# Performance work log

Hardware: AMD Instinct MI355X
Metric: run time of the kernel (lower is better)

Reference implementation:

```python
import jax, jax.numpy as jnp
import numpy as np

N = 1
IN_C = 256
NUM_ANCHORS = 9
NUM_CLASSES = 91
# (H, W, stride) per FPN level for an 800x800 input
LEVELS = [(100, 100, 8), (50, 50, 16), (25, 25, 32), (13, 13, 64), (7, 7, 128)]
BBOX_CLAMP = float(np.log(1000.0 / 16.0))


def setup_inputs() -> dict:
    key = jax.random.key(0)
    ks = jax.random.split(key, 12)
    std = 0.01
    inp = {}
    for i, (h, w, _) in enumerate(LEVELS):
        inp[f"feat{i}"] = jax.random.normal(ks[i], (N, IN_C, h, w), jnp.float32)
    inp["cls_tw"] = jax.random.normal(ks[5], (4, IN_C, IN_C, 3, 3), jnp.float32) * std
    inp["cls_tb"] = jnp.zeros((4, IN_C), jnp.float32)
    inp["cls_out_w"] = jax.random.normal(ks[6], (NUM_ANCHORS * NUM_CLASSES, IN_C, 3, 3), jnp.float32) * std
    # prior-probability bias init: -log((1-p)/p) with p=0.01
    inp["cls_out_b"] = jnp.full((NUM_ANCHORS * NUM_CLASSES,), -np.log((1 - 0.01) / 0.01), jnp.float32)
    inp["reg_tw"] = jax.random.normal(ks[7], (4, IN_C, IN_C, 3, 3), jnp.float32) * std
    inp["reg_tb"] = jnp.zeros((4, IN_C), jnp.float32)
    inp["reg_out_w"] = jax.random.normal(ks[8], (NUM_ANCHORS * 4, IN_C, 3, 3), jnp.float32) * std
    inp["reg_out_b"] = jnp.zeros((NUM_ANCHORS * 4,), jnp.float32)
    return inp


def _conv3(x, w, b):
    y = jax.lax.conv_general_dilated(x, w, (1, 1), [(1, 1), (1, 1)],
                                     dimension_numbers=("NCHW", "OIHW", "NCHW"))
    return y + b[None, :, None, None]


def _run_head(feat, tw, tb, ow, ob, K):
    x = feat
    for i in range(4):  # fixed 4-layer tower
        x = jax.nn.relu(_conv3(x, tw[i], tb[i]))
    y = _conv3(x, ow, ob)                      # [N, A*K, H, W]
    n, _, h, w = y.shape
    y = y.reshape(n, -1, K, h, w)              # [N, A, K, H, W]
    y = jnp.transpose(y, (0, 3, 4, 1, 2))      # [N, H, W, A, K]
    return y.reshape(n, -1, K)                 # [N, H*W*A, K]


def _make_anchors():
    base_sizes = [32.0, 64.0, 128.0, 256.0, 512.0]
    scales = np.array([2 ** (i / 3.0) for i in range(3)], np.float32)
    ratios = np.array([0.5, 1.0, 2.0], np.float32)
    h_ratios = np.sqrt(ratios)
    w_ratios = 1.0 / h_ratios
    out = []
    for lvl, (H, W, stride) in enumerate(LEVELS):
        sizes = base_sizes[lvl] * scales                      # [3]
        ws = (w_ratios[:, None] * sizes[None, :]).reshape(-1)  # [9], ratio-major
        hs = (h_ratios[:, None] * sizes[None, :]).reshape(-1)
        base = np.stack([-ws, -hs, ws, hs], axis=1) / 2.0      # [9, 4]
        sy = np.arange(H, dtype=np.float32) * stride
        sx = np.arange(W, dtype=np.float32) * stride
        yy, xx = np.meshgrid(sy, sx, indexing="ij")
        shifts = np.stack([xx, yy, xx, yy], axis=-1).reshape(-1, 4)  # [H*W, 4]
        out.append((shifts[:, None, :] + base[None, :, :]).reshape(-1, 4))
    return jnp.asarray(np.concatenate(out, axis=0))  # [A_total, 4]


def _decode(reg, anchors):
    # torchvision BoxCoder.decode with weights (1,1,1,1)
    aw = anchors[:, 2] - anchors[:, 0]
    ah = anchors[:, 3] - anchors[:, 1]
    acx = anchors[:, 0] + 0.5 * aw
    acy = anchors[:, 1] + 0.5 * ah
    dx, dy, dw, dh = reg[..., 0], reg[..., 1], reg[..., 2], reg[..., 3]
    dw = jnp.minimum(dw, BBOX_CLAMP)
    dh = jnp.minimum(dh, BBOX_CLAMP)
    pcx = dx * aw + acx
    pcy = dy * ah + acy
    pw = jnp.exp(dw) * aw
    ph = jnp.exp(dh) * ah
    return jnp.stack([pcx - 0.5 * pw, pcy - 0.5 * ph, pcx + 0.5 * pw, pcy + 0.5 * ph], axis=-1)


def reference(feat0, feat1, feat2, feat3, feat4,
              cls_tw, cls_tb, cls_out_w, cls_out_b,
              reg_tw, reg_tb, reg_out_w, reg_out_b):
    feats = [feat0, feat1, feat2, feat3, feat4]
    cls_logits = jnp.concatenate(
        [_run_head(f, cls_tw, cls_tb, cls_out_w, cls_out_b, NUM_CLASSES) for f in feats], axis=1)
    bbox_reg = jnp.concatenate(
        [_run_head(f, reg_tw, reg_tb, reg_out_w, reg_out_b, 4) for f in feats], axis=1)
    anchors = _make_anchors()                     # [A_total, 4]
    boxes = _decode(bbox_reg, anchors)            # [N, A_total, 4]
    scores = jax.nn.sigmoid(cls_logits)           # [N, A_total, 91]
    return jnp.concatenate([scores, boxes], axis=-1)  # [N, A_total, 95]
```

## Files before the change

kernel.cpp:

```cpp
#include <hip/hip_runtime.h>
#include <math.h>

typedef unsigned short u16;
typedef __attribute__((ext_vector_type(8))) short s8v;
typedef __attribute__((ext_vector_type(4))) float f4v;

#define NUM_CLASSES 91
#define NUM_ANCHORS 9
#define NT2 247
#define TG8 31
#define TW_STRIDE (256*256*9)
#define PSTRIDE 872

struct Tab {
    int tstart[5];
    int tw[5];
    int H[5], W[5], GP0[5];
};

__device__ __forceinline__ u16 f2bf(float f) {
    unsigned u = __float_as_uint(f);
    u += 0x7fffu + ((u >> 16) & 1u);
    return (u16)(u >> 16);
}

__global__ __launch_bounds__(256) void conv2bf_all(
    const float* __restrict__ f0, const float* __restrict__ f1,
    const float* __restrict__ f2, const float* __restrict__ f3,
    const float* __restrict__ f4, u16* __restrict__ out, Tab tab)
{
    int gp = blockIdx.x * 64 + (threadIdx.x & 63);
    int cg = threadIdx.x >> 6;
    if (gp >= 13343) return;
    int lvl = 0;
    if (gp >= tab.GP0[1]) lvl = 1;
    if (gp >= tab.GP0[2]) lvl = 2;
    if (gp >= tab.GP0[3]) lvl = 3;
    if (gp >= tab.GP0[4]) lvl = 4;
    const float* x = lvl == 0 ? f0 : lvl == 1 ? f1 : lvl == 2 ? f2 : lvl == 3 ? f3 : f4;
    int p = gp - tab.GP0[lvl];
    int HW = tab.H[lvl] * tab.W[lvl];
    #pragma unroll
    for (int pass = 0; pass < 8; ++pass) {
        int c0 = pass * 32 + cg * 8;
        s8v v8;
        #pragma unroll
        for (int j = 0; j < 8; ++j)
            v8[j] = (short)f2bf(x[(c0 + j) * HW + p]);
        *(s8v*)(out + (((size_t)gp << 8) + c0)) = v8;
    }
}

__device__ __forceinline__ void pack_one(const float* __restrict__ w,
                                         u16* __restrict__ dst,
                                         int idx, int c_out_real)
{
    int lane = idx & 63;
    int t2 = idx >> 6;
    int chunk = t2 % 72;
    int co16 = t2 / 72;
    int tap = chunk >> 3, cib = chunk & 7;
    int co = co16 * 16 + (lane & 15);
    int ci0 = cib * 32 + ((lane >> 4) << 3);
    s8v v8;
    #pragma unroll
    for (int j = 0; j < 8; ++j) {
        float v = (co < c_out_real) ? w[((co << 8) + ci0 + j) * 9 + tap] : 0.f;
        v8[j] = (short)f2bf(v);
    }
    *(s8v*)(dst + (size_t)idx * 8) = v8;
}

__global__ __launch_bounds__(256) void pack_all(
    const float* __restrict__ cls_tw, const float* __restrict__ reg_tw,
    const float* __restrict__ cls_ow, const float* __restrict__ reg_ow,
    u16* __restrict__ pt, size_t pt_stride_u16,
    u16* __restrict__ pc, u16* __restrict__ pr)
{
    int idx = blockIdx.x * 256 + threadIdx.x;
    const int per_t = 72 * 16 * 64;
    const int cls_n = 72 * 52 * 64;
    const int reg_n = 72 * 3 * 64;
    if (idx < 8 * per_t) {
        int layer = idx / per_t;
        int r = idx - layer * per_t;
        const float* src = (layer < 4) ? cls_tw + (size_t)layer * TW_STRIDE
                                       : reg_tw + (size_t)(layer - 4) * TW_STRIDE;
        pack_one(src, pt + (size_t)layer * pt_stride_u16, r, 256);
    } else if (idx < 8 * per_t + cls_n) {
        pack_one(cls_ow, pc, idx - 8 * per_t, 819);
    } else if (idx < 8 * per_t + cls_n + reg_n) {
        pack_one(reg_ow, pr, idx - 8 * per_t - cls_n, 36);
    }
}

__global__ __launch_bounds__(256) void pack_w(const float* __restrict__ w,
                                              u16* __restrict__ dst,
                                              int c_out_real, int nco16)
{
    int idx = blockIdx.x * 256 + threadIdx.x;
    if (idx < 72 * nco16 * 64) pack_one(w, dst, idx, c_out_real);
}

template<int MODE, int NCO16, int ACCN>
__device__ __forceinline__ void conv_core(
    u16* __restrict__ lds,
    const u16* __restrict__ act, const u16* __restrict__ wpk,
    const float* __restrict__ bias,
    u16* __restrict__ outw, float* __restrict__ fout,
    int bx, int by, const Tab& tab)
{
    int lvl = 0;
    if (by >= tab.tstart[1]) lvl = 1;
    if (by >= tab.tstart[2]) lvl = 2;
    if (by >= tab.tstart[3]) lvl = 3;
    if (by >= tab.tstart[4]) lvl = 4;
    const int H = tab.H[lvl], W = tab.W[lvl], gp0 = tab.GP0[lvl];
    const int t = by - tab.tstart[lvl];
    const int tw = tab.tw[lvl];
    const int w0 = (t % tw) * 16;
    const int h0 = (t / tw) * 4;

    const int tid = threadIdx.x;
    const int lane = tid & 63, wv = tid >> 6;
    const int co16w = bx * (4 * ACCN) + wv * ACCN;
    const int kg = lane >> 4;
    const int col = lane & 15;

    int sofs[4], slds[4];
    bool svalid[4], slive[4];
    #pragma unroll
    for (int i = 0; i < 4; ++i) {
        int k = tid + i * 256;
        slive[i] = k < 864;
        int kk = slive[i] ? k : 0;
        int px = kk >> 3, part = kk & 7;
        int hh = px / 18, ww = px - hh * 18;
        int gh = h0 + hh - 1, gw = w0 + ww - 1;
        svalid[i] = ((unsigned)gh < (unsigned)H) && ((unsigned)gw < (unsigned)W);
        sofs[i] = ((gp0 + gh * W + gw) << 8) + part * 8;
        slds[i] = part * PSTRIDE + px * 8;
    }

    const u16* bbn[ACCN];
    #pragma unroll
    for (int n = 0; n < ACCN; ++n) {
        int c = co16w + n;
        if (c >= NCO16) c = NCO16 - 1;
        bbn[n] = wpk + ((size_t)(c * 72) << 9) + (lane << 3);
    }

    f4v acc[4][ACCN];
    #pragma unroll
    for (int s = 0; s < 4; ++s)
        #pragma unroll
        for (int n = 0; n < ACCN; ++n)
            acc[s][n] = (f4v){0.f, 0.f, 0.f, 0.f};

    s8v pre[4];
    auto ISSUE_S = [&](int cc) {
        #pragma unroll
        for (int i = 0; i < 4; ++i) {
            s8v v = {};
            if (slive[i] && svalid[i])
                v = *(const s8v*)(act + sofs[i] + cc * 64);
            pre[i] = v;
        }
    };

    ISSUE_S(0);
    #pragma unroll 1
    for (int cib = 0; cib < 4; ++cib) {
        if (cib) __syncthreads();
        #pragma unroll
        for (int i = 0; i < 4; ++i)
            if (slive[i]) *(s8v*)(&lds[slds[i]]) = pre[i];
        __syncthreads();

        #pragma unroll
        for (int cs = 0; cs < 2; ++cs) {
            const u16* L = &lds[(cs * 4 + kg) * PSTRIDE];
            #pragma unroll
            for (int kx = 0; kx < 3; ++kx) {
                s8v a[6];
                #pragma unroll
                for (int r = 0; r < 6; ++r)
                    a[r] = *(const s8v*)(&L[(r * 18 + col + kx) * 8]);
                #pragma unroll
                for (int ky = 0; ky < 3; ++ky) {
                    s8v b[ACCN];
                    #pragma unroll
                    for (int n = 0; n < ACCN; ++n)
                        b[n] = *(const s8v*)(bbn[n] +
                            ((size_t)((ky * 3 + kx) * 8 + cib * 2 + cs) << 9));
                    #pragma unroll
                    for (int s = 0; s < 4; ++s)
                        #pragma unroll
                        for (int n = 0; n < ACCN; ++n)
                            acc[s][n] = __builtin_amdgcn_mfma_f32_16x16x32_bf16(
                                a[s + ky], b[n], acc[s][n], 0, 0, 0);
                }
                if (cs == 0 && kx == 0 && cib < 3) ISSUE_S(cib + 1);
            }
        }
    }

    #pragma unroll
    for (int n = 0; n < ACCN; ++n) {
        const int co = (co16w + n) * 16 + (lane & 15);
        if (co < NCO16 * 16) {
            #pragma unroll
            for (int s = 0; s < 4; ++s) {
                const int h = h0 + s;
                #pragma unroll
                for (int j = 0; j < 4; ++j) {
                    const int w = w0 + ((lane >> 4) << 2) + j;
                    if (h < H && w < W) {
                        const int p = h * W + w;
                        if (MODE == 0) {
                            float v = acc[s][n][j] + bias[co];
                            outw[((size_t)(gp0 + p) << 8) + co] = f2bf(fmaxf(v, 0.f));
                        } else if (MODE == 1) {
                            if (co < NUM_ANCHORS * NUM_CLASSES) {
                                float v = acc[s][n][j] + bias[co];
                                int a = co / NUM_CLASSES;
                                int k = co - a * NUM_CLASSES;
                                float sg = 1.f / (1.f + __expf(-v));
                                fout[((size_t)(gp0 + p) * 9 + a) * 95 + k] = sg;
                            }
                        } else {
                            if (co < 36)
                                fout[(gp0 + p) * 48 + co] = acc[s][n][j] + bias[co];
                        }
                    }
                }
            }
        }
    }
}


__global__ __launch_bounds__(256, 4) void conv_tower(
    const u16* __restrict__ actC, u16* __restrict__ outC,
    const u16* __restrict__ actR, u16* __restrict__ outR,
    const u16* __restrict__ wC, const u16* __restrict__ wR,
    const float* __restrict__ bC, const float* __restrict__ bR, Tab tab)
{
    __shared__ u16 lds[8 * PSTRIDE];
    const int s = blockIdx.x;
    const int xcd = s & 7;
    const int q = s >> 3;
    const int pass = q & 1;
    const int head = (q >> 1) & 1;
    const int t = (q >> 2) * 8 + xcd;
    if (t >= NT2) return;
    conv_core<0, 16, 2>(lds, head ? actR : actC, head ? wR : wC,
                        head ? bR : bC, head ? outR : outC, nullptr,
                        pass, t, tab);
}

__global__ __launch_bounds__(256, 4) void conv_cls(
    const u16* __restrict__ actD, const u16* __restrict__ wPC,
    const float* __restrict__ cls_ob, float* __restrict__ out, Tab tab)
{
    __shared__ u16 lds[8 * PSTRIDE];
    const int s = blockIdx.x;
    const int xcd = s & 7;
    const int q = s >> 3;
    const int pass = q % 7;
    const int t = (q / 7) * 8 + xcd;
    if (t >= NT2) return;
    conv_core<1, 52, 2>(lds, actD, wPC, cls_ob, nullptr, out, pass, t, tab);
}

__global__ __launch_bounds__(256, 4) void conv_reg(
    const u16* __restrict__ actA, const u16* __restrict__ wPR,
    const float* __restrict__ reg_ob, float* __restrict__ raw, Tab tab)
{
    __shared__ u16 lds[8 * PSTRIDE];
    conv_core<2, 3, 1>(lds, actA, wPR, reg_ob, nullptr, raw,
                       0, blockIdx.x, tab);
}

__global__ __launch_bounds__(256) void decode_boxes(
    const float* __restrict__ raw, float* __restrict__ out, Tab tab)
{
    int idx = blockIdx.x * 256 + threadIdx.x;
    if (idx >= 13343 * 9) return;
    int gp = idx / 9, a = idx % 9;
    int lvl = 0;
    if (gp >= tab.GP0[1]) lvl = 1;
    if (gp >= tab.GP0[2]) lvl = 2;
    if (gp >= tab.GP0[3]) lvl = 3;
    if (gp >= tab.GP0[4]) lvl = 4;
    int p = gp - tab.GP0[lvl];
    int W = tab.W[lvl];
    int h = p / W, wc = p % W;
    float stride = (float)(8 << lvl);
    float base = (float)(32 << lvl);

    float dx = raw[gp * 48 + a * 4 + 0];
    float dy = raw[gp * 48 + a * 4 + 1];
    float dw = raw[gp * 48 + a * 4 + 2];
    float dh = raw[gp * 48 + a * 4 + 3];

    const float scales[3] = {1.f, 1.2599210498948732f, 1.5874010519681994f};
    const float hr[3] = {0.70710678118654752f, 1.f, 1.41421356237309505f};
    int ri = a / 3, si = a % 3;
    float sz = base * scales[si];
    float ah = hr[ri] * sz;
    float aw = sz / hr[ri];
    float acx = (float)wc * stride;
    float acy = (float)h * stride;

    const float CLAMP = 4.135166556742356f;
    dw = fminf(dw, CLAMP);
    dh = fminf(dh, CLAMP);
    float pcx = dx * aw + acx;
    float pcy = dy * ah + acy;
    float pw = expf(dw) * aw;
    float ph = expf(dh) * ah;

    float* o = out + ((size_t)gp * 9 + a) * 95 + 91;
    o[0] = pcx - 0.5f * pw;
    o[1] = pcy - 0.5f * ph;
    o[2] = pcx + 0.5f * pw;
    o[3] = pcy + 0.5f * ph;
}

extern "C" void kernel_launch(void* const* d_in, const int* in_sizes, int n_in,
                              void* d_out, int out_size, void* d_ws, size_t ws_size,
                              hipStream_t stream)
{
    const float* f0 = (const float*)d_in[0];
    const float* f1 = (const float*)d_in[1];
    const float* f2 = (const float*)d_in[2];
    const float* f3 = (const float*)d_in[3];
    const float* f4 = (const float*)d_in[4];
    const float* cls_tw = (const float*)d_in[5];
    const float* cls_tb = (const float*)d_in[6];
    const float* cls_ow = (const float*)d_in[7];
    const float* cls_ob = (const float*)d_in[8];
    const float* reg_tw = (const float*)d_in[9];
    const float* reg_tb = (const float*)d_in[10];
    const float* reg_ow = (const float*)d_in[11];
    const float* reg_ob = (const float*)d_in[12];
    float* out = (float*)d_out;

    static const Tab TAB = {
        {0, 175, 227, 241, 245},
        {7, 4, 2, 1, 1},
        {100, 50, 25, 13, 7},
        {100, 50, 25, 13, 7},
        {0, 10000, 12500, 13125, 13294}
    };

    char* wsb = (char*)d_ws;
    const size_t AS = 6832128;
    u16* A = (u16*)(wsb + 0 * AS);
    u16* B = (u16*)(wsb + 1 * AS);
    u16* C = (u16*)(wsb + 2 * AS);
    u16* D = (u16*)(wsb + 3 * AS);
    float* RAW = (float*)B;

    const u16* cin[4]   = {A, B, D, B};
    u16*       cout_[4] = {B, D, B, D};
    const u16* rin[4]   = {A, C, A, C};
    u16*       rout[4]  = {C, A, C, A};

    const size_t PTSZ = 1179648;
    const bool big = ws_size >= (4 * AS + 8 * PTSZ + 3833856 + 221184);

    const int GT = 8 * 2 * 2 * TG8;
    const int GC = 8 * 7 * TG8;

    conv2bf_all<<<(13343 + 63) / 64, 256, 0, stream>>>(f0, f1, f2, f3, f4, A, TAB);

    if (big) {
        u16* PT = (u16*)(wsb + 4 * AS);
        u16* PC = (u16*)(wsb + 4 * AS + 8 * PTSZ);
        u16* PR = (u16*)(wsb + 4 * AS + 8 * PTSZ + 3833856);

        const int pack_total = 8 * 72 * 16 * 64 + 72 * 52 * 64 + 72 * 3 * 64;
        pack_all<<<(pack_total + 255) / 256, 256, 0, stream>>>(
            cls_tw, reg_tw, cls_ow, reg_ow, PT, PTSZ / 2, PC, PR);

        for (int s = 0; s < 4; ++s)
            conv_tower<<<GT, 256, 0, stream>>>(
                cin[s], cout_[s], rin[s], rout[s],
                PT + (size_t)s * (PTSZ / 2), PT + (size_t)(4 + s) * (PTSZ / 2),
                cls_tb + s * 256, reg_tb + s * 256, TAB);

        conv_cls<<<GC, 256, 0, stream>>>(D, PC, cls_ob, out, TAB);
        conv_reg<<<NT2, 256, 0, stream>>>(A, PR, reg_ob, RAW, TAB);
    } else {
        u16* PC = (u16*)(wsb + 4 * AS);
        u16* PR = (u16*)(wsb + 4 * AS + 3833856);
        for (int s = 0; s < 4; ++s) {
            pack_w<<<(72 * 16 * 64 + 255) / 256, 256, 0, stream>>>(cls_tw + s * TW_STRIDE, PC, 256, 16);
            pack_w<<<(72 * 16 * 64 + 255) / 256, 256, 0, stream>>>(reg_tw + s * TW_STRIDE, PR, 256, 16);
            conv_tower<<<GT, 256, 0, stream>>>(
                cin[s], cout_[s], rin[s], rout[s], PC, PR,
                cls_tb + s * 256, reg_tb + s * 256, TAB);
        }
        pack_w<<<(72 * 52 * 64 + 255) / 256, 256, 0, stream>>>(cls_ow, PC, 819, 52);
        conv_cls<<<GC, 256, 0, stream>>>(D, PC, cls_ob, out, TAB);
        pack_w<<<(72 * 3 * 64 + 255) / 256, 256, 0, stream>>>(reg_ow, PR, 36, 3);
        conv_reg<<<NT2, 256, 0, stream>>>(A, PR, reg_ob, RAW, TAB);
    }

    decode_boxes<<<(13343 * 9 + 255) / 256, 256, 0, stream>>>(RAW, out, TAB);
}
```

Measured before the change: 306.9 us.

## Stage conv input tiles via direct global-to-LDS loads with double buffering and XOR swizzle

Input halo tiles are now copied straight from global memory into LDS with global_load_lds instead of passing through registers. LDS is double-buffered so the next channel block loads while MFMAs run on the current one, and the layout uses an XOR swizzle in place of the padded stride to avoid bank conflicts. Out-of-bounds pixels read from a small zero buffer that conv2bf_all writes into the workspace. This cuts register pressure and one barrier per iteration, at the cost of more LDS per block, which may lower occupancy. It also relies on the async LDS loads having completed when the barrier is reached.

Result: slower. 438.1 us (+42.8%).

```diff
diff --git a/kernel.cpp b/kernel.cpp
--- a/kernel.cpp
+++ b/kernel.cpp
@@ -10,7 +10,7 @@
 #define NT2 247
 #define TG8 31
 #define TW_STRIDE (256*256*9)
-#define PSTRIDE 872
+#define ZB_OFF 6831616
 
 struct Tab {
     int tstart[5];
@@ -27,8 +27,11 @@
 __global__ __launch_bounds__(256) void conv2bf_all(
     const float* __restrict__ f0, const float* __restrict__ f1,
     const float* __restrict__ f2, const float* __restrict__ f3,
-    const float* __restrict__ f4, u16* __restrict__ out, Tab tab)
-{
+    const float* __restrict__ f4, u16* __restrict__ out,
+    float* __restrict__ zb, Tab tab)
+{
+    if (blockIdx.x == 0 && threadIdx.x < 128)
+        zb[threadIdx.x] = 0.f;
     int gp = blockIdx.x * 64 + (threadIdx.x & 63);
     int cg = threadIdx.x >> 6;
     if (gp >= 13343) return;
@@ -104,9 +107,9 @@
 
 template<int MODE, int NCO16, int ACCN>
 __device__ __forceinline__ void conv_core(
-    u16* __restrict__ lds,
+    u16* __restrict__ lds0,
     const u16* __restrict__ act, const u16* __restrict__ wpk,
-    const float* __restrict__ bias,
+    const float* __restrict__ bias, const u16* __restrict__ zb,
     u16* __restrict__ outw, float* __restrict__ fout,
     int bx, int by, const Tab& tab)
 {
@@ -127,19 +130,19 @@
     const int kg = lane >> 4;
     const int col = lane & 15;
 
-    int sofs[4], slds[4];
-    bool svalid[4], slive[4];
+    const u16* sptr[4];
+    bool svalid[4];
     #pragma unroll
     for (int i = 0; i < 4; ++i) {
         int k = tid + i * 256;
-        slive[i] = k < 864;
-        int kk = slive[i] ? k : 0;
-        int px = kk >> 3, part = kk & 7;
+        int px = k >> 3;
+        int part = (k & 7) ^ (px & 7);
         int hh = px / 18, ww = px - hh * 18;
         int gh = h0 + hh - 1, gw = w0 + ww - 1;
-        svalid[i] = ((unsigned)gh < (unsigned)H) && ((unsigned)gw < (unsigned)W);
-        sofs[i] = ((gp0 + gh * W + gw) << 8) + part * 8;
-        slds[i] = part * PSTRIDE + px * 8;
+        bool v = (px < 108) && ((unsigned)gh < (unsigned)H) &&
+                 ((unsigned)gw < (unsigned)W);
+        svalid[i] = v;
+        sptr[i] = v ? act + ((gp0 + gh * W + gw) << 8) + part * 8 : zb;
     }
 
     const u16* bbn[ACCN];
@@ -157,35 +160,37 @@
         for (int n = 0; n < ACCN; ++n)
             acc[s][n] = (f4v){0.f, 0.f, 0.f, 0.f};
 
-    s8v pre[4];
-    auto ISSUE_S = [&](int cc) {
+    auto STAGE = [&](int buf, int cc) {
         #pragma unroll
         for (int i = 0; i < 4; ++i) {
-            s8v v = {};
-            if (slive[i] && svalid[i])
-                v = *(const s8v*)(act + sofs[i] + cc * 64);
-            pre[i] = v;
+            const u16* s = svalid[i] ? sptr[i] + cc * 64 : sptr[i];
+            __builtin_amdgcn_global_load_lds(
+                (const __attribute__((address_space(1))) void*)s,
+                (__attribute__((address_space(3))) void*)
+                    (lds0 + (size_t)buf * 8192 + (wv * 64 + i * 256) * 8),
+                16, 0, 0);
         }
     };
 
-    ISSUE_S(0);
+    STAGE(0, 0);
+    __syncthreads();
+    int cur = 0;
     #pragma unroll 1
     for (int cib = 0; cib < 4; ++cib) {
-        if (cib) __syncthreads();
-        #pragma unroll
-        for (int i = 0; i < 4; ++i)
-            if (slive[i]) *(s8v*)(&lds[slds[i]]) = pre[i];
-        __syncthreads();
+        if (cib < 3) STAGE(cur ^ 1, cib + 1);
+        const u16* L = lds0 + (size_t)cur * 8192;
 
         #pragma unroll
         for (int cs = 0; cs < 2; ++cs) {
-            const u16* L = &lds[(cs * 4 + kg) * PSTRIDE];
+            const int p = cs * 4 + kg;
             #pragma unroll
             for (int kx = 0; kx < 3; ++kx) {
                 s8v a[6];
                 #pragma unroll
-                for (int r = 0; r < 6; ++r)
-                    a[r] = *(const s8v*)(&L[(r * 18 + col + kx) * 8]);
+                for (int r = 0; r < 6; ++r) {
+                    int px = r * 18 + col + kx;
+                    a[r] = *(const s8v*)(&L[(px << 6) + ((p ^ (px & 7)) << 3)]);
+                }
                 #pragma unroll
                 for (int ky = 0; ky < 3; ++ky) {
                     s8v b[ACCN];
@@ -200,9 +205,10 @@
                             acc[s][n] = __builtin_amdgcn_mfma_f32_16x16x32_bf16(
                                 a[s + ky], b[n], acc[s][n], 0, 0, 0);
                 }
-                if (cs == 0 && kx == 0 && cib < 3) ISSUE_S(cib + 1);
             }
         }
+        __syncthreads();
+        cur ^= 1;
     }
 
     #pragma unroll
@@ -244,9 +250,10 @@
     const u16* __restrict__ actC, u16* __restrict__ outC,
     const u16* __restrict__ actR, u16* __restrict__ outR,
     const u16* __restrict__ wC, const u16* __restrict__ wR,
-    const float* __restrict__ bC, const float* __restrict__ bR, Tab tab)
-{
-    __shared__ u16 lds[8 * PSTRIDE];
+    const float* __restrict__ bC, const float* __restrict__ bR,
+    const u16* __restrict__ zb, Tab tab)
+{
+    __shared__ u16 lds[2 * 8192];
     const int s = blockIdx.x;
     const int xcd = s & 7;
     const int q = s >> 3;
@@ -255,30 +262,32 @@
     const int t = (q >> 2) * 8 + xcd;
     if (t >= NT2) return;
     conv_core<0, 16, 2>(lds, head ? actR : actC, head ? wR : wC,
-                        head ? bR : bC, head ? outR : outC, nullptr,
+                        head ? bR : bC, zb, head ? outR : outC, nullptr,
                         pass, t, tab);
 }
 
 __global__ __launch_bounds__(256, 4) void conv_cls(
     const u16* __restrict__ actD, const u16* __restrict__ wPC,
-    const float* __restrict__ cls_ob, float* __restrict__ out, Tab tab)
-{
-    __shared__ u16 lds[8 * PSTRIDE];
+    const float* __restrict__ cls_ob, const u16* __restrict__ zb,
+    float* __restrict__ out, Tab tab)
+{
+    __shared__ u16 lds[2 * 8192];
     const int s = blockIdx.x;
     const int xcd = s & 7;
     const int q = s >> 3;
     const int pass = q % 7;
     const int t = (q / 7) * 8 + xcd;
     if (t >= NT2) return;
-    conv_core<1, 52, 2>(lds, actD, wPC, cls_ob, nullptr, out, pass, t, tab);
+    conv_core<1, 52, 2>(lds, actD, wPC, cls_ob, zb, nullptr, out, pass, t, tab);
 }
 
 __global__ __launch_bounds__(256, 4) void conv_reg(
     const u16* __restrict__ actA, const u16* __restrict__ wPR,
-    const float* __restrict__ reg_ob, float* __restrict__ raw, Tab tab)
-{
-    __shared__ u16 lds[8 * PSTRIDE];
-    conv_core<2, 3, 1>(lds, actA, wPR, reg_ob, nullptr, raw,
+    const float* __restrict__ reg_ob, const u16* __restrict__ zb,
+    float* __restrict__ raw, Tab tab)
+{
+    __shared__ u16 lds[2 * 8192];
+    conv_core<2, 3, 1>(lds, actA, wPR, reg_ob, zb, nullptr, raw,
                        0, blockIdx.x, tab);
 }
 
@@ -362,6 +371,7 @@
     u16* C = (u16*)(wsb + 2 * AS);
     u16* D = (u16*)(wsb + 3 * AS);
     float* RAW = (float*)B;
+    const u16* ZB = (const u16*)(wsb + ZB_OFF);
 
     const u16* cin[4]   = {A, B, D, B};
     u16*       cout_[4] = {B, D, B, D};
@@ -374,7 +384,8 @@
     const int GT = 8 * 2 * 2 * TG8;
     const int GC = 8 * 7 * TG8;
 
-    conv2bf_all<<<(13343 + 63) / 64, 256, 0, stream>>>(f0, f1, f2, f3, f4, A, TAB);
+    conv2bf_all<<<(13343 + 63) / 64, 256, 0, stream>>>(
+        f0, f1, f2, f3, f4, A, (float*)(wsb + ZB_OFF), TAB);
 
     if (big) {
         u16* PT = (u16*)(wsb + 4 * AS);
@@ -389,10 +400,10 @@
             conv_tower<<<GT, 256, 0, stream>>>(
                 cin[s], cout_[s], rin[s], rout[s],
                 PT + (size_t)s * (PTSZ / 2), PT + (size_t)(4 + s) * (PTSZ / 2),
-                cls_tb + s * 256, reg_tb + s * 256, TAB);
-
-        conv_cls<<<GC, 256, 0, stream>>>(D, PC, cls_ob, out, TAB);
-        conv_reg<<<NT2, 256, 0, stream>>>(A, PR, reg_ob, RAW, TAB);
+                cls_tb + s * 256, reg_tb + s * 256, ZB, TAB);
+
+        conv_cls<<<GC, 256, 0, stream>>>(D, PC, cls_ob, ZB, out, TAB);
+        conv_reg<<<NT2, 256, 0, stream>>>(A, PR, reg_ob, ZB, RAW, TAB);
     } else {
         u16* PC = (u16*)(wsb + 4 * AS);
         u16* PR = (u16*)(wsb + 4 * AS + 3833856);
@@ -401,12 +412,12 @@
             pack_w<<<(72 * 16 * 64 + 255) / 256, 256, 0, stream>>>(reg_tw + s * TW_STRIDE, PR, 256, 16);
             conv_tower<<<GT, 256, 0, stream>>>(
                 cin[s], cout_[s], rin[s], rout[s], PC, PR,
-                cls_tb + s * 256, reg_tb + s * 256, TAB);
+                cls_tb + s * 256, reg_tb + s * 256, ZB, TAB);
         }
         pack_w<<<(72 * 52 * 64 + 255) / 256, 256, 0, stream>>>(cls_ow, PC, 819, 52);
-        conv_cls<<<GC, 256, 0, stream>>>(D, PC, cls_ob, out, TAB);
+        conv_cls<<<GC, 256, 0, stream>>>(D, PC, cls_ob, ZB, out, TAB);
         pack_w<<<(72 * 3 * 64 + 255) / 256, 256, 0, stream>>>(reg_ow, PR, 36, 3);
-        conv_reg<<<NT2, 256, 0, stream>>>(A, PR, reg_ob, RAW, TAB);
+        conv_reg<<<NT2, 256, 0, stream>>>(A, PR, reg_ob, ZB, RAW, TAB);
     }
 
     decode_boxes<<<(13343 * 9 + 255) / 256, 256, 0, stream>>>(RAW, out, TAB);
```

## Stage conv epilogues through LDS for coalesced stores and merge cls/reg output kernels

Applied to the files above, without the earlier changes.

The tower conv epilogue now writes bias+ReLU bf16 results into LDS and then has each thread store contiguous 16-byte channel vectors per pixel, replacing scattered 2-byte global stores. The class-output epilogue likewise transposes fp32 logits through LDS in two halves so sigmoid outputs are written per pixel row with better locality. The separate cls and reg output-conv launches are merged into one grid, with the reg work as an eighth pass, which removes a launch and lets the small reg conv overlap the cls conv. The cost is extra LDS traffic and __syncthreads, plus a new LDS size and layout.

Result: slower. 328.5 us (+7.0%).

```diff
diff --git a/kernel.cpp b/kernel.cpp
--- a/kernel.cpp
+++ b/kernel.cpp
@@ -205,33 +205,88 @@
         }
     }
 
-    #pragma unroll
-    for (int n = 0; n < ACCN; ++n) {
-        const int co = (co16w + n) * 16 + (lane & 15);
-        if (co < NCO16 * 16) {
+    if (MODE == 0) {
+        __syncthreads();
+        #pragma unroll
+        for (int n = 0; n < ACCN; ++n) {
+            const int co_l = ((wv * ACCN + n) << 4) + col;
+            const float bval = bias[bx * 128 + co_l];
             #pragma unroll
-            for (int s = 0; s < 4; ++s) {
-                const int h = h0 + s;
+            for (int s = 0; s < 4; ++s)
                 #pragma unroll
                 for (int j = 0; j < 4; ++j) {
-                    const int w = w0 + ((lane >> 4) << 2) + j;
-                    if (h < H && w < W) {
-                        const int p = h * W + w;
-                        if (MODE == 0) {
-                            float v = acc[s][n][j] + bias[co];
-                            outw[((size_t)(gp0 + p) << 8) + co] = f2bf(fmaxf(v, 0.f));
-                        } else if (MODE == 1) {
-                            if (co < NUM_ANCHORS * NUM_CLASSES) {
-                                float v = acc[s][n][j] + bias[co];
-                                int a = co / NUM_CLASSES;
-                                int k = co - a * NUM_CLASSES;
-                                float sg = 1.f / (1.f + __expf(-v));
-                                fout[((size_t)(gp0 + p) * 9 + a) * 95 + k] = sg;
-                            }
-                        } else {
-                            if (co < 36)
-                                fout[(gp0 + p) * 48 + co] = acc[s][n][j] + bias[co];
+                    int px = (s << 4) + ((lane >> 4) << 2) + j;
+                    float v = acc[s][n][j] + bval;
+                    lds[px * 136 + co_l] = f2bf(fmaxf(v, 0.f));
+                }
+        }
+        __syncthreads();
+        const int px = tid >> 2, q = tid & 3;
+        const int r = px >> 4, c = px & 15;
+        const int gh = h0 + r, gw = w0 + c;
+        if (gh < H && gw < W) {
+            const u16* src = &lds[px * 136 + (q << 5)];
+            u16* dst = outw + (((size_t)(gp0 + gh * W + gw)) << 8)
+                            + bx * 128 + (q << 5);
+            #pragma unroll
+            for (int c4 = 0; c4 < 4; ++c4)
+                *(s8v*)(dst + c4 * 8) = *(const s8v*)(src + c4 * 8);
+        }
+    } else if (MODE == 1) {
+        float* Tf = (float*)lds;
+        #pragma unroll
+        for (int hf = 0; hf < 2; ++hf) {
+            __syncthreads();
+            #pragma unroll
+            for (int n = 0; n < ACCN; ++n) {
+                const int co_l = ((wv * ACCN + n) << 4) + col;
+                const int co = bx * 128 + co_l;
+                const float bval = (co < 819) ? bias[co] : 0.f;
+                #pragma unroll
+                for (int s2 = 0; s2 < 2; ++s2)
+                    #pragma unroll
+                    for (int j = 0; j < 4; ++j) {
+                        int px32 = (s2 << 4) + ((lane >> 4) << 2) + j;
+                        Tf[px32 * 132 + co_l] = acc[hf * 2 + s2][n][j] + bval;
+                    }
+            }
+            __syncthreads();
+            const int px32 = tid >> 3, q = tid & 7;
+            const int px = hf * 32 + px32;
+            const int r = px >> 4, c = px & 15;
+            const int gh = h0 + r, gw = w0 + c;
+            if (gh < H && gw < W) {
+                float* rowb = fout + (size_t)(gp0 + gh * W + gw) * 855;
+                const float* src = &Tf[px32 * 132 + (q << 4)];
+                #pragma unroll
+                for (int c4 = 0; c4 < 4; ++c4) {
+                    f4v v4 = *(const f4v*)(src + (c4 << 2));
+                    #pragma unroll
+                    for (int i = 0; i < 4; ++i) {
+                        int co = bx * 128 + (q << 4) + (c4 << 2) + i;
+                        if (co < NUM_ANCHORS * NUM_CLASSES) {
+                            int a = co / NUM_CLASSES;
+                            int k = co - a * NUM_CLASSES;
+                            float sg = 1.f / (1.f + __expf(-v4[i]));
+                            rowb[a * 95 + k] = sg;
                         }
+                    }
+                }
+            }
+        }
+    } else {
+        #pragma unroll
+        for (int n = 0; n < ACCN; ++n) {
+            const int co = (co16w + n) * 16 + col;
+            if (co < 36) {
+                #pragma unroll
+                for (int s = 0; s < 4; ++s) {
+                    const int h = h0 + s;
+                    #pragma unroll
+                    for (int j = 0; j < 4; ++j) {
+                        const int w = w0 + ((lane >> 4) << 2) + j;
+                        if (h < H && w < W)
+                            fout[(gp0 + h * W + w) * 48 + co] = acc[s][n][j] + bias[co];
                     }
                 }
             }
@@ -246,7 +301,7 @@
     const u16* __restrict__ wC, const u16* __restrict__ wR,
     const float* __restrict__ bC, const float* __restrict__ bR, Tab tab)
 {
-    __shared__ u16 lds[8 * PSTRIDE];
+    __shared__ __align__(16) u16 lds[8704];
     const int s = blockIdx.x;
     const int xcd = s & 7;
     const int q = s >> 3;
@@ -259,27 +314,23 @@
                         pass, t, tab);
 }
 
-__global__ __launch_bounds__(256, 4) void conv_cls(
-    const u16* __restrict__ actD, const u16* __restrict__ wPC,
-    const float* __restrict__ cls_ob, float* __restrict__ out, Tab tab)
-{
-    __shared__ u16 lds[8 * PSTRIDE];
+__global__ __launch_bounds__(256, 4) void conv_out(
+    const u16* __restrict__ actD, const u16* __restrict__ actA,
+    const u16* __restrict__ wPC, const u16* __restrict__ wPR,
+    const float* __restrict__ cls_ob, const float* __restrict__ reg_ob,
+    float* __restrict__ out, float* __restrict__ raw, Tab tab)
+{
+    __shared__ __align__(16) u16 lds[8448];
     const int s = blockIdx.x;
     const int xcd = s & 7;
     const int q = s >> 3;
-    const int pass = q % 7;
-    const int t = (q / 7) * 8 + xcd;
+    const int pass = q & 7;
+    const int t = (q >> 3) * 8 + xcd;
     if (t >= NT2) return;
-    conv_core<1, 52, 2>(lds, actD, wPC, cls_ob, nullptr, out, pass, t, tab);
-}
-
-__global__ __launch_bounds__(256, 4) void conv_reg(
-    const u16* __restrict__ actA, const u16* __restrict__ wPR,
-    const float* __restrict__ reg_ob, float* __restrict__ raw, Tab tab)
-{
-    __shared__ u16 lds[8 * PSTRIDE];
-    conv_core<2, 3, 1>(lds, actA, wPR, reg_ob, nullptr, raw,
-                       0, blockIdx.x, tab);
+    if (pass < 7)
+        conv_core<1, 52, 2>(lds, actD, wPC, cls_ob, nullptr, out, pass, t, tab);
+    else
+        conv_core<2, 3, 1>(lds, actA, wPR, reg_ob, nullptr, raw, 0, t, tab);
 }
 
 __global__ __launch_bounds__(256) void decode_boxes(
@@ -372,7 +423,7 @@
     const bool big = ws_size >= (4 * AS + 8 * PTSZ + 3833856 + 221184);
 
     const int GT = 8 * 2 * 2 * TG8;
-    const int GC = 8 * 7 * TG8;
+    const int GO = 8 * 8 * TG8;
 
     conv2bf_all<<<(13343 + 63) / 64, 256, 0, stream>>>(f0, f1, f2, f3, f4, A, TAB);
 
@@ -391,8 +442,7 @@
                 PT + (size_t)s * (PTSZ / 2), PT + (size_t)(4 + s) * (PTSZ / 2),
                 cls_tb + s * 256, reg_tb + s * 256, TAB);
 
-        conv_cls<<<GC, 256, 0, stream>>>(D, PC, cls_ob, out, TAB);
-        conv_reg<<<NT2, 256, 0, stream>>>(A, PR, reg_ob, RAW, TAB);
+        conv_out<<<GO, 256, 0, stream>>>(D, A, PC, PR, cls_ob, reg_ob, out, RAW, TAB);
     } else {
         u16* PC = (u16*)(wsb + 4 * AS);
         u16* PR = (u16*)(wsb + 4 * AS + 3833856);
@@ -404,9 +454,8 @@
                 cls_tb + s * 256, reg_tb + s * 256, TAB);
         }
         pack_w<<<(72 * 52 * 64 + 255) / 256, 256, 0, stream>>>(cls_ow, PC, 819, 52);
-        conv_cls<<<GC, 256, 0, stream>>>(D, PC, cls_ob, out, TAB);
         pack_w<<<(72 * 3 * 64 + 255) / 256, 256, 0, stream>>>(reg_ow, PR, 36, 3);
-        conv_reg<<<NT2, 256, 0, stream>>>(A, PR, reg_ob, RAW, TAB);
+        conv_out<<<GO, 256, 0, stream>>>(D, A, PC, PR, cls_ob, reg_ob, out, RAW, TAB);
     }
 
     decode_boxes<<<(13343 * 9 + 255) / 256, 256, 0, stream>>>(RAW, out, TAB);
```

## Use 512-thread tower blocks covering all 256 output channels per tile

Applied to the files above, without the earlier changes.

The tower conv kernel now launches 512-thread blocks (8 waves) so that one block computes all 16 output-channel groups for a spatial tile, instead of two 256-thread blocks each handling half the channels. This halves the grid and means each input tile is staged into LDS once rather than twice, reducing redundant activation loads and staging work. The trade-off is fewer blocks for the GPU to schedule and larger blocks with more barrier participants. Launch bounds of (512,4) may also force tighter register limits.

Measured after the change: 294.6 us. -4.0%, faster.

```diff
diff --git a/kernel.cpp b/kernel.cpp
--- a/kernel.cpp
+++ b/kernel.cpp
@@ -102,7 +102,7 @@
     if (idx < 72 * nco16 * 64) pack_one(w, dst, idx, c_out_real);
 }
 
-template<int MODE, int NCO16, int ACCN>
+template<int MODE, int NCO16, int ACCN, int NTHR>
 __device__ __forceinline__ void conv_core(
     u16* __restrict__ lds,
     const u16* __restrict__ act, const u16* __restrict__ wpk,
@@ -110,6 +110,9 @@
     u16* __restrict__ outw, float* __restrict__ fout,
     int bx, int by, const Tab& tab)
 {
+    constexpr int NW = NTHR / 64;
+    constexpr int SJOBS = (864 + NTHR - 1) / NTHR;
+
     int lvl = 0;
     if (by >= tab.tstart[1]) lvl = 1;
     if (by >= tab.tstart[2]) lvl = 2;
@@ -123,15 +126,15 @@
 
     const int tid = threadIdx.x;
     const int lane = tid & 63, wv = tid >> 6;
-    const int co16w = bx * (4 * ACCN) + wv * ACCN;
+    const int co16w = bx * (NW * ACCN) + wv * ACCN;
     const int kg = lane >> 4;
     const int col = lane & 15;
 
-    int sofs[4], slds[4];
-    bool svalid[4], slive[4];
-    #pragma unroll
-    for (int i = 0; i < 4; ++i) {
-        int k = tid + i * 256;
+    int sofs[SJOBS], slds[SJOBS];
+    bool svalid[SJOBS], slive[SJOBS];
+    #pragma unroll
+    for (int i = 0; i < SJOBS; ++i) {
+        int k = tid + i * NTHR;
         slive[i] = k < 864;
         int kk = slive[i] ? k : 0;
         int px = kk >> 3, part = kk & 7;
@@ -157,10 +160,10 @@
         for (int n = 0; n < ACCN; ++n)
             acc[s][n] = (f4v){0.f, 0.f, 0.f, 0.f};
 
-    s8v pre[4];
+    s8v pre[SJOBS];
     auto ISSUE_S = [&](int cc) {
         #pragma unroll
-        for (int i = 0; i < 4; ++i) {
+        for (int i = 0; i < SJOBS; ++i) {
             s8v v = {};
             if (slive[i] && svalid[i])
                 v = *(const s8v*)(act + sofs[i] + cc * 64);
@@ -173,7 +176,7 @@
     for (int cib = 0; cib < 4; ++cib) {
         if (cib) __syncthreads();
         #pragma unroll
-        for (int i = 0; i < 4; ++i)
+        for (int i = 0; i < SJOBS; ++i)
             if (slive[i]) *(s8v*)(&lds[slds[i]]) = pre[i];
         __syncthreads();
 
@@ -240,7 +243,7 @@
 }
 
 
-__global__ __launch_bounds__(256, 4) void conv_tower(
+__global__ __launch_bounds__(512, 4) void conv_tower(
     const u16* __restrict__ actC, u16* __restrict__ outC,
     const u16* __restrict__ actR, u16* __restrict__ outR,
     const u16* __restrict__ wC, const u16* __restrict__ wR,
@@ -250,13 +253,12 @@
     const int s = blockIdx.x;
     const int xcd = s & 7;
     const int q = s >> 3;
-    const int pass = q & 1;
-    const int head = (q >> 1) & 1;
-    const int t = (q >> 2) * 8 + xcd;
+    const int head = q & 1;
+    const int t = (q >> 1) * 8 + xcd;
     if (t >= NT2) return;
-    conv_core<0, 16, 2>(lds, head ? actR : actC, head ? wR : wC,
-                        head ? bR : bC, head ? outR : outC, nullptr,
-                        pass, t, tab);
+    conv_core<0, 16, 2, 512>(lds, head ? actR : actC, head ? wR : wC,
+                             head ? bR : bC, head ? outR : outC, nullptr,
+                             0, t, tab);
 }
 
 __global__ __launch_bounds__(256, 4) void conv_cls(
@@ -270,7 +272,7 @@
     const int pass = q % 7;
     const int t = (q / 7) * 8 + xcd;
     if (t >= NT2) return;
-    conv_core<1, 52, 2>(lds, actD, wPC, cls_ob, nullptr, out, pass, t, tab);
+    conv_core<1, 52, 2, 256>(lds, actD, wPC, cls_ob, nullptr, out, pass, t, tab);
 }
 
 __global__ __launch_bounds__(256, 4) void conv_reg(
@@ -278,8 +280,8 @@
     const float* __restrict__ reg_ob, float* __restrict__ raw, Tab tab)
 {
     __shared__ u16 lds[8 * PSTRIDE];
-    conv_core<2, 3, 1>(lds, actA, wPR, reg_ob, nullptr, raw,
-                       0, blockIdx.x, tab);
+    conv_core<2, 3, 1, 256>(lds, actA, wPR, reg_ob, nullptr, raw,
+                            0, blockIdx.x, tab);
 }
 
 __global__ __launch_bounds__(256) void decode_boxes(
@@ -371,7 +373,7 @@
     const size_t PTSZ = 1179648;
     const bool big = ws_size >= (4 * AS + 8 * PTSZ + 3833856 + 221184);
 
-    const int GT = 8 * 2 * 2 * TG8;
+    const int GT = 8 * 2 * TG8;
     const int GC = 8 * 7 * TG8;
 
     conv2bf_all<<<(13343 + 63) / 64, 256, 0, stream>>>(f0, f1, f2, f3, f4, A, TAB);
@@ -386,7 +388,7 @@
             cls_tw, reg_tw, cls_ow, reg_ow, PT, PTSZ / 2, PC, PR);
 
         for (int s = 0; s < 4; ++s)
-            conv_tower<<<GT, 256, 0, stream>>>(
+            conv_tower<<<GT, 512, 0, stream>>>(
                 cin[s], cout_[s], rin[s], rout[s],
                 PT + (size_t)s * (PTSZ / 2), PT + (size_t)(4 + s) * (PTSZ / 2),
                 cls_tb + s * 256, reg_tb + s * 256, TAB);
@@ -399,7 +401,7 @@
         for (int s = 0; s < 4; ++s) {
             pack_w<<<(72 * 16 * 64 + 255) / 256, 256, 0, stream>>>(cls_tw + s * TW_STRIDE, PC, 256, 16);
             pack_w<<<(72 * 16 * 64 + 255) / 256, 256, 0, stream>>>(reg_tw + s * TW_STRIDE, PR, 256, 16);
-            conv_tower<<<GT, 256, 0, stream>>>(
+            conv_tower<<<GT, 512, 0, stream>>>(
                 cin[s], cout_[s], rin[s], rout[s], PC, PR,
                 cls_tb + s * 256, reg_tb + s * 256, TAB);
         }
```
